# Optimization experiments

Hardware: AMD Instinct MI355X
Metric: run time of the kernel (lower is better)

## Reference

```python
import jax, jax.numpy as jnp
import numpy as np

N = 1_000_000          # points
C_IN = 10              # decorated point features
C_OUT = 64             # pillar feature channels
S = 30_000             # number of pillars (segments)
EPS = 1e-3             # BatchNorm1d eps


def setup_inputs() -> dict:
    key = jax.random.key(0)
    ks = jax.random.split(key, 8)
    inputs = jax.random.normal(ks[0], (N, C_IN), dtype=jnp.float32)
    # every pillar gets ~N/S points; sorted, all segments non-empty
    unq_inv = jnp.sort(jnp.arange(N, dtype=jnp.int32) % S)
    W_lin = jax.random.normal(ks[1], (C_OUT, C_IN), dtype=jnp.float32) * 0.3
    gamma = 1.0 + 0.1 * jax.random.normal(ks[2], (C_OUT,), dtype=jnp.float32)
    beta = 0.1 * jax.random.normal(ks[3], (C_OUT,), dtype=jnp.float32)
    dw1 = jax.random.normal(ks[4], (C_OUT,), dtype=jnp.float32) * 0.5      # depthwise 1x1 conv (groups=C)
    pw1 = jax.random.normal(ks[5], (C_OUT, C_OUT), dtype=jnp.float32) * 0.1  # pointwise 1x1 conv
    dw2 = jax.random.normal(ks[6], (C_OUT,), dtype=jnp.float32) * 0.5
    pw2 = jax.random.normal(ks[7], (C_OUT, C_OUT), dtype=jnp.float32) * 0.1
    return {"inputs": inputs, "unq_inv": unq_inv, "W_lin": W_lin,
            "gamma": gamma, "beta": beta, "dw1": dw1, "pw1": pw1,
            "dw2": dw2, "pw2": pw2}


def reference(inputs, unq_inv, W_lin, gamma, beta, dw1, pw1, dw2, pw2):
    # Linear (no bias) -> BN (training-mode batch stats) -> ReLU
    x = inputs @ W_lin.T                                   # [N, C]
    mu = jnp.mean(x, axis=0)
    var = jnp.mean(jnp.square(x - mu), axis=0)             # biased var, as torch BN
    x = (x - mu) * jax.lax.rsqrt(var + EPS) * gamma + beta
    x = jax.nn.relu(x)

    # MAFF attention: local branch (depthwise scale -> swish -> 1x1 conv)
    s = x * dw1                                            # groups=C 1x1 conv == per-channel scale
    xl = (s * jax.nn.sigmoid(s)) @ pw1.T                   # [N, C]
    # global branch: avg-pool over points -> depthwise scale -> relu -> 1x1 conv
    g = jnp.mean(x, axis=0)                                # [C]
    xg = pw2 @ jax.nn.relu(dw2 * g)                        # [C]
    wei = jax.nn.sigmoid(xl + xg)                          # broadcast [N,C] + [C]
    xi = x * (1.0 + wei)

    # segment reductions keyed by pillar id (scatter_max + scatter_sum)
    x_max = jax.ops.segment_max(xi, unq_inv, num_segments=S,
                                indices_are_sorted=True)
    x_sum = jax.ops.segment_sum(xi, unq_inv, num_segments=S,
                                indices_are_sorted=True)
    return x_max + x_sum                                   # [S, C]
```

## Files before the change

### kernel.cpp

```cpp
#include <hip/hip_runtime.h>
#include <math.h>

#define N_PTS   1000000
#define CI      10
#define C       64
#define NSEG    30000
#define BN_EPS  1e-3f
#define FROFF   31104


using f32x4 = __attribute__((ext_vector_type(4))) float;
using s16x8 = __attribute__((ext_vector_type(8))) short;

__device__ inline short f2bf(float x) {
    unsigned u = __float_as_uint(x);
    unsigned r = (u + 0x7fffu + ((u >> 16) & 1u)) >> 16;
    return (short)r;
}
__device__ inline unsigned pack_trunc(float lo, float hi) {
    return (__float_as_uint(hi) & 0xffff0000u) | (__float_as_uint(lo) >> 16);
}
__device__ inline float frcp(float x) { return __builtin_amdgcn_rcpf(x); }

__global__ void __launch_bounds__(256) k_moments(const float* __restrict__ inp,
                                                 const int* __restrict__ idx,
                                                 float* __restrict__ ws,
                                                 int* __restrict__ starts) {
    const int tid = threadIdx.x;
    float v[65];
#pragma unroll
    for (int k = 0; k < 65; ++k) v[k] = 0.f;

    for (int p = blockIdx.x * blockDim.x + tid; p < N_PTS; p += gridDim.x * blockDim.x) {
        const float2* r2 = (const float2*)(inp + (size_t)p * CI);
        float2 a0 = r2[0], a1 = r2[1], a2 = r2[2], a3 = r2[3], a4 = r2[4];
        float r[CI] = {a0.x, a0.y, a1.x, a1.y, a2.x, a2.y, a3.x, a3.y, a4.x, a4.y};
#pragma unroll
        for (int i = 0; i < CI; ++i) v[i] += r[i];
        int kk = 10;
#pragma unroll
        for (int i = 0; i < CI; ++i)
#pragma unroll
            for (int j = i; j < CI; ++j) { v[kk] = fmaf(r[i], r[j], v[kk]); ++kk; }

        int iv = idx[p];
        if (p == 0) starts[0] = 0;
        else if (idx[p - 1] != iv) starts[iv] = p;
    }

#pragma unroll
    for (int k = 0; k < 65; ++k) {
#pragma unroll
        for (int off = 32; off >= 1; off >>= 1)
            v[k] += __shfl_xor(v[k], off, 64);
    }
    __shared__ float red[4 * 65];
    const int wv = tid >> 6, ln = tid & 63;
    if (ln == 0) {
#pragma unroll
        for (int k = 0; k < 65; ++k) red[wv * 65 + k] = v[k];
    }
    __syncthreads();
    if (tid < 65)
        atomicAdd(&ws[tid], red[tid] + red[65 + tid] + red[130 + tid] + red[195 + tid]);
}

__global__ void __launch_bounds__(256) k_gstats(const float* __restrict__ inp,
                                                const float* __restrict__ W,
                                                const float* __restrict__ gamma,
                                                const float* __restrict__ beta,
                                                float* __restrict__ ws) {
    const int tid  = threadIdx.x;
    const int wv   = tid >> 6;
    const int lane = tid & 63;
    const int m = lane & 15;
    const int q = lane >> 4;

    __shared__ float wp[C * CI];
    __shared__ float bsh[C];

    if (tid < C) {
        const int c = tid;
        float w[CI];
#pragma unroll
        for (int i = 0; i < CI; ++i) w[i] = W[c * CI + i];
        const float inv_n = 1.f / (float)N_PTS;

        float mu = 0.f;
#pragma unroll
        for (int i = 0; i < CI; ++i) mu = fmaf(w[i], ws[i], mu);
        mu *= inv_n;

        float ex2 = 0.f;
        int kk = 10;
#pragma unroll
        for (int i = 0; i < CI; ++i)
#pragma unroll
            for (int j = i; j < CI; ++j) {
                float mm = ws[kk];
                float t = w[i] * w[j] * mm;
                ex2 += (i == j) ? t : 2.f * t;
                ++kk;
            }
        ex2 *= inv_n;

        float var = ex2 - mu * mu;
        float rstd = rsqrtf(var + BN_EPS);
        float a = rstd * gamma[c];
        float b = beta[c] - mu * a;
        bsh[c] = b;
        ws[128 + c] = a;
        ws[192 + c] = b;
#pragma unroll
        for (int i = 0; i < CI; ++i) {
            float wi = a * w[i];
            wp[c * CI + i] = wi;
            ws[384 + c * CI + i] = wi;
        }
    }
    __syncthreads();

    s16x8 wfr[4];
#pragma unroll
    for (int nt = 0; nt < 4; ++nt) {
        s16x8 t;
#pragma unroll
        for (int j = 0; j < 8; ++j) {
            int k = 8 * q + j;
            t[j] = (k < CI) ? f2bf(wp[(nt * 16 + m) * CI + k]) : (short)0;
        }
        wfr[nt] = t;
    }
    float bb[4];
#pragma unroll
    for (int nt = 0; nt < 4; ++nt) bb[nt] = bsh[nt * 16 + m];

    const int wid = blockIdx.x * 4 + wv;
    const int nw  = gridDim.x * 4;
    const int NB  = N_PTS / 16;

    float2 P0, P1, P2, P3;
    auto loadrows = [&](int pb) {
        const float* row = inp + (size_t)(pb + m) * CI;
        if (q == 0) {
            P0 = *(const float2*)(row);     P1 = *(const float2*)(row + 2);
            P2 = *(const float2*)(row + 4); P3 = *(const float2*)(row + 6);
        } else if (q == 1) {
            P0 = *(const float2*)(row + 8);
        }
    };
    P0 = P1 = P2 = P3 = make_float2(0.f, 0.f);

    float sm[4] = {0.f, 0.f, 0.f, 0.f};
    const f32x4 zero = {0.f, 0.f, 0.f, 0.f};

    if (wid < NB) loadrows(wid * 16);
    for (int b = wid; b < NB; b += nw) {
        float2 L0 = P0, L1 = P1, L2 = P2, L3 = P3;
        if (b + nw < NB) loadrows((b + nw) * 16);

        union { s16x8 v; unsigned u[4]; } t;
        t.v = s16x8{0, 0, 0, 0, 0, 0, 0, 0};
        if (q < 2) t.u[0] = pack_trunc(L0.x, L0.y);
        if (q == 0) {
            t.u[1] = pack_trunc(L1.x, L1.y);
            t.u[2] = pack_trunc(L2.x, L2.y);
            t.u[3] = pack_trunc(L3.x, L3.y);
        }

        f32x4 xt[4];
#pragma unroll
        for (int nt = 0; nt < 4; ++nt) {
            xt[nt] = __builtin_amdgcn_mfma_f32_16x16x32_bf16(t.v, wfr[nt], zero, 0, 0, 0);
#pragma unroll
            for (int r = 0; r < 4; ++r)
                sm[nt] += fmaxf(xt[nt][r] + bb[nt], 0.f);
        }
    }

#pragma unroll
    for (int nt = 0; nt < 4; ++nt) {
        sm[nt] += __shfl_xor(sm[nt], 16, 64);
        sm[nt] += __shfl_xor(sm[nt], 32, 64);
    }
    float S = sm[0];
    if (q == 1) S = sm[1];
    if (q == 2) S = sm[2];
    if (q == 3) S = sm[3];

    __shared__ float red[4 * 64];
    red[wv * 64 + lane] = S;
    __syncthreads();
    if (tid < 64)
        atomicAdd(&ws[256 + tid], red[tid] + red[64 + tid] + red[128 + tid] + red[192 + tid]);
}

__global__ void k_prep(const float* __restrict__ dw1,
                       const float* __restrict__ pw1,
                       const float* __restrict__ dw2,
                       const float* __restrict__ pw2,
                       float* __restrict__ ws) {
    const int lane = threadIdx.x;
    const int m = lane & 15, q = lane >> 4;
    __shared__ float t[C], xgs[C];
    const float inv_n = 1.f / (float)N_PTS;
    t[lane] = fmaxf(dw2[lane] * (ws[256 + lane] * inv_n), 0.f);
    __syncthreads();
    float acc = 0.f;
#pragma unroll
    for (int k = 0; k < C; ++k) acc = fmaf(pw2[lane * C + k], t[k], acc);
    xgs[lane] = acc;
    __syncthreads();

    float4* FR = (float4*)(ws + FROFF);
    union { float4 f; s16x8 v; } u;

#pragma unroll
    for (int nt = 0; nt < 4; ++nt) {
        s16x8 tt;
#pragma unroll
        for (int j = 0; j < 8; ++j) {
            int k = 8 * q + j;
            tt[j] = (k < CI) ? f2bf(ws[384 + (nt * 16 + m) * CI + k]) : (short)0;
        }
        u.v = tt; FR[nt * 64 + lane] = u.f;
    }
#pragma unroll
    for (int nt = 0; nt < 4; ++nt)
#pragma unroll
        for (int kc = 0; kc < 2; ++kc) {
            const float* src = pw1 + (nt * 16 + m) * C + kc * 32 + q * 8;
            float4 p0 = *(const float4*)src, p1 = *(const float4*)(src + 4);
            s16x8 tt;
            tt[0] = f2bf(p0.x); tt[1] = f2bf(p0.y); tt[2] = f2bf(p0.z); tt[3] = f2bf(p0.w);
            tt[4] = f2bf(p1.x); tt[5] = f2bf(p1.y); tt[6] = f2bf(p1.z); tt[7] = f2bf(p1.w);
            u.v = tt; FR[(4 + nt * 2 + kc) * 64 + lane] = u.f;
        }
    float4 f;
    f.x = ws[192 + m]; f.y = ws[192 + 16 + m]; f.z = ws[192 + 32 + m]; f.w = ws[192 + 48 + m];
    FR[12 * 64 + lane] = f;
    f.x = dw1[m]; f.y = dw1[16 + m]; f.z = dw1[32 + m]; f.w = dw1[48 + m];
    FR[13 * 64 + lane] = f;
    f.x = xgs[m]; f.y = xgs[16 + m]; f.z = xgs[32 + m]; f.w = xgs[48 + m];
    FR[14 * 64 + lane] = f;
}

#define LD 68
#define SEGW 2
__global__ void __launch_bounds__(128) k_main(const float* __restrict__ inp,
                                              const float* __restrict__ ws,
                                              const int* __restrict__ starts,
                                              float* __restrict__ out) {
    const int tid  = threadIdx.x;
    const int wv   = tid >> 6;
    const int lane = tid & 63;
    const int m = lane & 15;
    const int q = lane >> 4;
    const f32x4 zero = {0.f, 0.f, 0.f, 0.f};

    const float4* FR = (const float4*)(ws + FROFF);
    union { float4 f; s16x8 v; } u;
    s16x8 wfr[4];
#pragma unroll
    for (int nt = 0; nt < 4; ++nt) { u.f = FR[nt * 64 + lane]; wfr[nt] = u.v; }
    s16x8 bfr[4][2];
#pragma unroll
    for (int nt = 0; nt < 4; ++nt)
#pragma unroll
        for (int kc = 0; kc < 2; ++kc) { u.f = FR[(4 + nt * 2 + kc) * 64 + lane]; bfr[nt][kc] = u.v; }
    const float4 bb4  = FR[12 * 64 + lane];
    const float4 d14  = FR[13 * 64 + lane];
    const float4 xg4  = FR[14 * 64 + lane];
    const float bb[4]  = {bb4.x, bb4.y, bb4.z, bb4.w};
    const float d1v[4] = {d14.x, d14.y, d14.z, d14.w};
    const float xgv[4] = {xg4.x, xg4.y, xg4.z, xg4.w};

    __shared__ float sb[2][16 * LD];
    float* my = sb[wv];

    const int w  = blockIdx.x * 2 + wv;
    const int s0 = w * SEGW;

    int st1 = starts[s0 + 1];
    int st2 = (s0 + 2 < NSEG) ? starts[s0 + 2] : N_PTS;
    const int start   = starts[s0];
    const int end_all = st2;

    int cur = s0;
    int end_cur = st1;

    float sm[4]  = {0.f, 0.f, 0.f, 0.f};
    float mxv[4] = {-INFINITY, -INFINITY, -INFINITY, -INFINITY};

    auto flushseg = [&](int s) {
#pragma unroll
        for (int nt = 0; nt < 4; ++nt) {
            sm[nt] += __shfl_xor(sm[nt], 16, 64);
            sm[nt] += __shfl_xor(sm[nt], 32, 64);
            mxv[nt] = fmaxf(mxv[nt], __shfl_xor(mxv[nt], 16, 64));
            mxv[nt] = fmaxf(mxv[nt], __shfl_xor(mxv[nt], 32, 64));
        }
        float S = sm[0], M = mxv[0];
        if (q == 1) { S = sm[1]; M = mxv[1]; }
        if (q == 2) { S = sm[2]; M = mxv[2]; }
        if (q == 3) { S = sm[3]; M = mxv[3]; }
        out[(size_t)s * C + lane] = S + M;
#pragma unroll
        for (int nt = 0; nt < 4; ++nt) { sm[nt] = 0.f; mxv[nt] = -INFINITY; }
    };

    float2 P0, P1, P2, P3;
    auto loadrows = [&](int pb) {
        const float* row = inp + (size_t)min(pb + m, N_PTS - 1) * CI;
        if (q == 0) {
            P0 = *(const float2*)(row);     P1 = *(const float2*)(row + 2);
            P2 = *(const float2*)(row + 4); P3 = *(const float2*)(row + 6);
        } else if (q == 1) {
            P0 = *(const float2*)(row + 8);
        }
    };
    P0 = P1 = P2 = P3 = make_float2(0.f, 0.f);
    loadrows(start);

    for (int base = start; base < end_all; base += 16) {
        float2 L0 = P0, L1 = P1, L2 = P2, L3 = P3;
        if (base + 16 < end_all) loadrows(base + 16);

        const int nb = min(16, end_all - base);

        union { s16x8 v; unsigned u[4]; } t;
        t.v = s16x8{0, 0, 0, 0, 0, 0, 0, 0};
        if (q < 2) t.u[0] = pack_trunc(L0.x, L0.y);
        if (q == 0) {
            t.u[1] = pack_trunc(L1.x, L1.y);
            t.u[2] = pack_trunc(L2.x, L2.y);
            t.u[3] = pack_trunc(L3.x, L3.y);
        }

        f32x4 xt[4];
#pragma unroll
        for (int nt = 0; nt < 4; ++nt)
            xt[nt] = __builtin_amdgcn_mfma_f32_16x16x32_bf16(t.v, wfr[nt], zero, 0, 0, 0);

        float xn[4][4];
#pragma unroll
        for (int nt = 0; nt < 4; ++nt)
#pragma unroll
            for (int r = 0; r < 4; ++r) {
                float x = fmaxf(xt[nt][r] + bb[nt], 0.f);
                xn[nt][r] = x;
                float sg = x * d1v[nt];
                float sw = sg * frcp(1.f + __expf(-sg));
                my[(4 * q + r) * LD + nt * 16 + m] = sw;
            }
        __threadfence_block();

        s16x8 av[2];
#pragma unroll
        for (int kc = 0; kc < 2; ++kc) {
            const float* src = &my[m * LD + kc * 32 + q * 8];
            float4 p0 = *(const float4*)src;
            float4 p1 = *(const float4*)(src + 4);
            union { s16x8 v; unsigned u[4]; } tt;
            tt.u[0] = pack_trunc(p0.x, p0.y);
            tt.u[1] = pack_trunc(p0.z, p0.w);
            tt.u[2] = pack_trunc(p1.x, p1.y);
            tt.u[3] = pack_trunc(p1.z, p1.w);
            av[kc] = tt.v;
        }

        f32x4 xi[4];
#pragma unroll
        for (int nt = 0; nt < 4; ++nt) {
            xi[nt] = __builtin_amdgcn_mfma_f32_16x16x32_bf16(av[0], bfr[nt][0], zero, 0, 0, 0);
            xi[nt] = __builtin_amdgcn_mfma_f32_16x16x32_bf16(av[1], bfr[nt][1], xi[nt], 0, 0, 0);
        }
        __threadfence_block();

#pragma unroll
        for (int nt = 0; nt < 4; ++nt)
#pragma unroll
            for (int r = 0; r < 4; ++r) {
                float v   = xi[nt][r] + xgv[nt];
                float wei = frcp(1.f + __expf(-v));
                float x   = xn[nt][r];
                xi[nt][r] = fmaf(x, wei, x);
            }

        const int fin = base + nb;
        if (fin <= end_cur) {
            if (nb == 16) {
#pragma unroll
                for (int nt = 0; nt < 4; ++nt)
#pragma unroll
                    for (int r = 0; r < 4; ++r) {
                        sm[nt] += xi[nt][r];
                        mxv[nt] = fmaxf(mxv[nt], xi[nt][r]);
                    }
            } else {
#pragma unroll
                for (int nt = 0; nt < 4; ++nt)
#pragma unroll
                    for (int r = 0; r < 4; ++r) {
                        bool act = (4 * q + r) < nb;
                        sm[nt] += act ? xi[nt][r] : 0.f;
                        mxv[nt] = fmaxf(mxv[nt], act ? xi[nt][r] : -INFINITY);
                    }
            }
            if (fin == end_cur) { flushseg(cur); ++cur; end_cur = st2; }
        } else {
            const int B = end_cur - base;
#pragma unroll
            for (int nt = 0; nt < 4; ++nt)
#pragma unroll
                for (int r = 0; r < 4; ++r) {
                    bool act = (4 * q + r) < B;
                    sm[nt] += act ? xi[nt][r] : 0.f;
                    mxv[nt] = fmaxf(mxv[nt], act ? xi[nt][r] : -INFINITY);
                }
            flushseg(cur); ++cur;
#pragma unroll
            for (int nt = 0; nt < 4; ++nt)
#pragma unroll
                for (int r = 0; r < 4; ++r) {
                    int pt = 4 * q + r;
                    bool act = (pt >= B) && (pt < nb);
                    sm[nt] += act ? xi[nt][r] : 0.f;
                    mxv[nt] = fmaxf(mxv[nt], act ? xi[nt][r] : -INFINITY);
                }
            end_cur = st2;
        }
    }
}

extern "C" void kernel_launch(void* const* d_in, const int* in_sizes, int n_in,
                              void* d_out, int out_size, void* d_ws, size_t ws_size,
                              hipStream_t stream) {
    const float* inp   = (const float*)d_in[0];
    const int*   unq   = (const int*)d_in[1];
    const float* W     = (const float*)d_in[2];
    const float* gamma = (const float*)d_in[3];
    const float* beta  = (const float*)d_in[4];
    const float* dw1   = (const float*)d_in[5];
    const float* pw1   = (const float*)d_in[6];
    const float* dw2   = (const float*)d_in[7];
    const float* pw2   = (const float*)d_in[8];
    float* out = (float*)d_out;
    float* ws  = (float*)d_ws;
    int* starts = (int*)ws + 1024;

    hipMemsetAsync(ws, 0, 384 * sizeof(float), stream);

    k_moments <<<1024, 256, 0, stream>>>(inp, unq, ws, starts);
    k_gstats  <<<1024, 256, 0, stream>>>(inp, W, gamma, beta, ws);
    k_prep    <<<1,    64,  0, stream>>>(dw1, pw1, dw2, pw2, ws);
    k_main    <<<7500, 128, 0, stream>>>(inp, ws, starts, out);
}
```

Measured before the change: 285.3 us.

## Deepen row prefetch to two tiles, lighten LDS fences, recompute BN params in prep

```diff
diff --git a/kernel.cpp b/kernel.cpp
--- a/kernel.cpp
+++ b/kernel.cpp
@@ -21,6 +21,9 @@
     return (__float_as_uint(hi) & 0xffff0000u) | (__float_as_uint(lo) >> 16);
 }
 __device__ inline float frcp(float x) { return __builtin_amdgcn_rcpf(x); }
+__device__ inline void lds_fence() {
+    asm volatile("s_waitcnt lgkmcnt(0)" ::: "memory");
+}
 
 __global__ void __launch_bounds__(256) k_moments(const float* __restrict__ inp,
                                                  const int* __restrict__ idx,
@@ -109,14 +112,8 @@
         float a = rstd * gamma[c];
         float b = beta[c] - mu * a;
         bsh[c] = b;
-        ws[128 + c] = a;
-        ws[192 + c] = b;
-#pragma unroll
-        for (int i = 0; i < CI; ++i) {
-            float wi = a * w[i];
-            wp[c * CI + i] = wi;
-            ws[384 + c * CI + i] = wi;
-        }
+#pragma unroll
+        for (int i = 0; i < CI; ++i) wp[c * CI + i] = a * w[i];
     }
     __syncthreads();
 
@@ -195,21 +192,57 @@
         atomicAdd(&ws[256 + tid], red[tid] + red[64 + tid] + red[128 + tid] + red[192 + tid]);
 }
 
-__global__ void k_prep(const float* __restrict__ dw1,
+__global__ void k_prep(const float* __restrict__ W,
+                       const float* __restrict__ gamma,
+                       const float* __restrict__ beta,
+                       const float* __restrict__ dw1,
                        const float* __restrict__ pw1,
                        const float* __restrict__ dw2,
                        const float* __restrict__ pw2,
                        float* __restrict__ ws) {
     const int lane = threadIdx.x;
     const int m = lane & 15, q = lane >> 4;
-    __shared__ float t[C], xgs[C];
     const float inv_n = 1.f / (float)N_PTS;
-    t[lane] = fmaxf(dw2[lane] * (ws[256 + lane] * inv_n), 0.f);
+
+    __shared__ float WP[C * CI];
+    __shared__ float BSH[C], T[C], XG[C];
+
+    {
+        float w[CI];
+#pragma unroll
+        for (int i = 0; i < CI; ++i) w[i] = W[lane * CI + i];
+        float mu = 0.f;
+#pragma unroll
+        for (int i = 0; i < CI; ++i) mu = fmaf(w[i], ws[i], mu);
+        mu *= inv_n;
+        float ex2 = 0.f;
+        int kk = 10;
+#pragma unroll
+        for (int i = 0; i < CI; ++i)
+#pragma unroll
+            for (int j = i; j < CI; ++j) {
+                float mm = ws[kk];
+                float t = w[i] * w[j] * mm;
+                ex2 += (i == j) ? t : 2.f * t;
+                ++kk;
+            }
+        ex2 *= inv_n;
+        float var = ex2 - mu * mu;
+        float rstd = rsqrtf(var + BN_EPS);
+        float a = rstd * gamma[lane];
+        BSH[lane] = beta[lane] - mu * a;
+#pragma unroll
+        for (int i = 0; i < CI; ++i) WP[lane * CI + i] = a * w[i];
+        T[lane] = fmaxf(dw2[lane] * (ws[256 + lane] * inv_n), 0.f);
+    }
     __syncthreads();
-    float acc = 0.f;
-#pragma unroll
-    for (int k = 0; k < C; ++k) acc = fmaf(pw2[lane * C + k], t[k], acc);
-    xgs[lane] = acc;
+
+    {
+        float acc = 0.f;
+#pragma unroll
+        for (int k = 0; k < C; ++k) acc = fmaf(pw2[lane * C + k], T[k], acc);
+        XG[lane] = acc;
+    }
     __syncthreads();
 
     float4* FR = (float4*)(ws + FROFF);
@@ -221,7 +254,7 @@
 #pragma unroll
         for (int j = 0; j < 8; ++j) {
             int k = 8 * q + j;
-            tt[j] = (k < CI) ? f2bf(ws[384 + (nt * 16 + m) * CI + k]) : (short)0;
+            tt[j] = (k < CI) ? f2bf(WP[(nt * 16 + m) * CI + k]) : (short)0;
         }
         u.v = tt; FR[nt * 64 + lane] = u.f;
     }
@@ -237,16 +270,17 @@
             u.v = tt; FR[(4 + nt * 2 + kc) * 64 + lane] = u.f;
         }
     float4 f;
-    f.x = ws[192 + m]; f.y = ws[192 + 16 + m]; f.z = ws[192 + 32 + m]; f.w = ws[192 + 48 + m];
+    f.x = BSH[m]; f.y = BSH[16 + m]; f.z = BSH[32 + m]; f.w = BSH[48 + m];
     FR[12 * 64 + lane] = f;
     f.x = dw1[m]; f.y = dw1[16 + m]; f.z = dw1[32 + m]; f.w = dw1[48 + m];
     FR[13 * 64 + lane] = f;
-    f.x = xgs[m]; f.y = xgs[16 + m]; f.z = xgs[32 + m]; f.w = xgs[48 + m];
+    f.x = XG[m]; f.y = XG[16 + m]; f.z = XG[32 + m]; f.w = XG[48 + m];
     FR[14 * 64 + lane] = f;
 }
 
 #define LD 68
 #define SEGW 2
+struct Rows { float2 r0, r1, r2, r3; };
 __global__ void __launch_bounds__(128) k_main(const float* __restrict__ inp,
                                               const float* __restrict__ ws,
                                               const int* __restrict__ starts,
@@ -309,32 +343,36 @@
         for (int nt = 0; nt < 4; ++nt) { sm[nt] = 0.f; mxv[nt] = -INFINITY; }
     };
 
-    float2 P0, P1, P2, P3;
-    auto loadrows = [&](int pb) {
+    auto loadrows = [&](int pb) -> Rows {
+        Rows R;
+        R.r0 = R.r1 = R.r2 = R.r3 = make_float2(0.f, 0.f);
         const float* row = inp + (size_t)min(pb + m, N_PTS - 1) * CI;
         if (q == 0) {
-            P0 = *(const float2*)(row);     P1 = *(const float2*)(row + 2);
-            P2 = *(const float2*)(row + 4); P3 = *(const float2*)(row + 6);
+            R.r0 = *(const float2*)(row);     R.r1 = *(const float2*)(row + 2);
+            R.r2 = *(const float2*)(row + 4); R.r3 = *(const float2*)(row + 6);
         } else if (q == 1) {
-            P0 = *(const float2*)(row + 8);
-        }
+            R.r0 = *(const float2*)(row + 8);
+        }
+        return R;
     };
-    P0 = P1 = P2 = P3 = make_float2(0.f, 0.f);
-    loadrows(start);
+
+    Rows A = loadrows(start);
+    Rows B = (start + 16 < end_all) ? loadrows(start + 16) : A;
 
     for (int base = start; base < end_all; base += 16) {
-        float2 L0 = P0, L1 = P1, L2 = P2, L3 = P3;
-        if (base + 16 < end_all) loadrows(base + 16);
+        Rows L = A;
+        A = B;
+        if (base + 32 < end_all) B = loadrows(base + 32);
 
         const int nb = min(16, end_all - base);
 
         union { s16x8 v; unsigned u[4]; } t;
         t.v = s16x8{0, 0, 0, 0, 0, 0, 0, 0};
-        if (q < 2) t.u[0] = pack_trunc(L0.x, L0.y);
+        if (q < 2) t.u[0] = pack_trunc(L.r0.x, L.r0.y);
         if (q == 0) {
-            t.u[1] = pack_trunc(L1.x, L1.y);
-            t.u[2] = pack_trunc(L2.x, L2.y);
-            t.u[3] = pack_trunc(L3.x, L3.y);
+            t.u[1] = pack_trunc(L.r1.x, L.r1.y);
+            t.u[2] = pack_trunc(L.r2.x, L.r2.y);
+            t.u[3] = pack_trunc(L.r3.x, L.r3.y);
         }
 
         f32x4 xt[4];
@@ -353,7 +391,7 @@
                 float sw = sg * frcp(1.f + __expf(-sg));
                 my[(4 * q + r) * LD + nt * 16 + m] = sw;
             }
-        __threadfence_block();
+        lds_fence();
 
         s16x8 av[2];
 #pragma unroll
@@ -375,7 +413,7 @@
             xi[nt] = __builtin_amdgcn_mfma_f32_16x16x32_bf16(av[0], bfr[nt][0], zero, 0, 0, 0);
             xi[nt] = __builtin_amdgcn_mfma_f32_16x16x32_bf16(av[1], bfr[nt][1], xi[nt], 0, 0, 0);
         }
-        __threadfence_block();
+        lds_fence();
 
 #pragma unroll
         for (int nt = 0; nt < 4; ++nt)
@@ -453,6 +491,6 @@
 
     k_moments <<<1024, 256, 0, stream>>>(inp, unq, ws, starts);
     k_gstats  <<<1024, 256, 0, stream>>>(inp, W, gamma, beta, ws);
-    k_prep    <<<1,    64,  0, stream>>>(dw1, pw1, dw2, pw2, ws);
+    k_prep    <<<1,    64,  0, stream>>>(W, gamma, beta, dw1, pw1, dw2, pw2, ws);
     k_main    <<<7500, 128, 0, stream>>>(inp, ws, starts, out);
 }
```

Result: faster. 268.2 us (-6.0%).
